# Kernel optimization log

Measured on AMD Instinct MI355X. Metric: run time of the kernel, lower is better.

## Reference

```python
import jax, jax.numpy as jnp
import numpy as np

PAD = 2  # kernel_height // 2 for kernel_height=5


def earth_pad2d(x, ph, pw):
    # circular pad in longitude (last dim), zero pad in latitude (dim 2)
    if pw > 0:
        x = jnp.concatenate([x[..., -pw:], x, x[..., :pw]], axis=-1)
    if ph > 0:
        x = jnp.pad(x, ((0, 0), (0, 0), (ph, ph), (0, 0)))
    return x


def earth_wrap2d(x, w, pad):
    # fold circular overhang of a transposed-conv output back onto width w
    core = x[..., pad:pad + w]
    rw = x.shape[-1] - pad - w  # right overhang (stride-1... here 1)
    core = core.at[..., :rw].add(x[..., pad + w:])
    core = core.at[..., w - pad:].add(x[..., :pad])
    return core


def _conv(x, w, b, stride):
    # torch Conv2d, weight [Cout, Cin, 1, k], VALID padding, stride (1, stride)
    y = jax.lax.conv_general_dilated(x, w, (1, stride), 'VALID',
                                     dimension_numbers=('NCHW', 'OIHW', 'NCHW'))
    return y + b[None, :, None, None]


def _convT(x, w, stride):
    # torch ConvTranspose2d (no bias), weight [Cin, Cout, 1, k], padding 0
    k = w.shape[-1]
    wr = jnp.transpose(jnp.flip(w, axis=(2, 3)), (1, 0, 2, 3))  # -> [Cout, Cin, 1, k]
    return jax.lax.conv_general_dilated(x, wr, (1, 1),
                                        [(0, 0), (k - 1, k - 1)],
                                        lhs_dilation=(1, stride),
                                        dimension_numbers=('NCHW', 'OIHW', 'NCHW'))


def _edge(x, d, p):
    return x[:, :, -p:, :] if d == 1 else x[:, :, :p, :]


def _set_edge(x, d, p, v):
    return x.at[:, :, -p:, :].set(v) if d == 1 else x.at[:, :, :p, :].set(v)


def _forward(strips, wi, wo):
    strips_pad = [earth_pad2d(s, PAD, PAD) for s in strips]
    # center strip inner edges from the adjacent coarser strips (to_inners[0])
    for d in (-1, 1):
        a = _edge(strips[2 + d], -d, PAD)
        a = _convT(a, wi[0], 2)
        a = earth_wrap2d(a, strips[2].shape[3], 2)
        a = earth_pad2d(a, 0, PAD)
        strips_pad[2] = _set_edge(strips_pad[2], d, PAD, a)
    # outer strips: far edge from next coarser (to_inners), near edge from finer (to_outers)
    for mi in (1, 2):
        for d in (-1, 1):
            idx = 2 + d * mi
            sp = strips_pad[idx]
            if mi + 1 <= 2:
                o = _edge(strips[2 + d * (mi + 1)], -d, PAD)
                o = _convT(o, wi[mi], 2)
                o = earth_wrap2d(o, strips[idx].shape[3], 2)
                o = earth_pad2d(o, 0, PAD)
                sp = _set_edge(sp, d, PAD, o)
            en = _edge(strips[2 + d * (mi - 1)], d, PAD)
            en = earth_pad2d(en, 0, 2)
            en = _conv(en, wo[mi - 1][0], wo[mi - 1][1], 2)
            en = earth_pad2d(en, 0, PAD)
            sp = _set_edge(sp, -d, PAD, en)
            strips_pad[idx] = sp
    return tuple(strips_pad)


def setup_inputs():
    key = jax.random.key(0)
    ks = jax.random.split(key, 11)
    B, C, W = 1, 256, 1440
    shapes = [(B, C, 30, W // 4), (B, C, 60, W // 2), (B, C, 180, W),
              (B, C, 60, W // 2), (B, C, 30, W // 4)]
    d = {}
    for i, sh in enumerate(shapes):
        d['s%d' % i] = jax.random.normal(ks[i], sh, dtype=jnp.float32)
    scale = 0.03
    d['wi0'] = jax.random.normal(ks[5], (C, C, 1, 5), dtype=jnp.float32) * scale
    d['wi1'] = jax.random.normal(ks[6], (C, C, 1, 5), dtype=jnp.float32) * scale
    d['wo0'] = jax.random.normal(ks[7], (C, C, 1, 5), dtype=jnp.float32) * scale
    d['bo0'] = jax.random.normal(ks[8], (C,), dtype=jnp.float32) * 0.01
    d['wo1'] = jax.random.normal(ks[9], (C, C, 1, 5), dtype=jnp.float32) * scale
    d['bo1'] = jax.random.normal(ks[10], (C,), dtype=jnp.float32) * 0.01
    return d


def reference(s0, s1, s2, s3, s4, wi0, wi1, wo0, bo0, wo1, bo1):
    return _forward([s0, s1, s2, s3, s4], [wi0, wi1], [(wo0, bo0), (wo1, bo1)])
```

## Files before the change

### kernel.cpp

```cpp
#include <hip/hip_runtime.h>


struct ConvJob {
  const float* x; const float* wt; const float* bias; float* out;
  int Hin, Win, r0, Hout, Wcore, h0, type, blk_start;
};

struct MegaParams {
  ConvJob j[8];
  const float* in0; const float* in1; const float* in2; const float* in3; const float* in4;
  float* o0; float* o1; float* o2; float* o3; float* o4;
};

struct WTParams { const float* src[4]; float* dst[4]; };

__global__ __launch_bounds__(256) void transpose_all_kernel(WTParams p) {
  int b = blockIdx.x;
  int which = b / 1280;
  int idx = (b - which * 1280) * 256 + threadIdx.x;
  int oc = idx & 255;
  int q = idx >> 8;
  int k = q % 5;
  int ic = q / 5;
  const float* s = p.src[which];
  float v = (which < 2) ? s[(ic * 256 + oc) * 5 + k] : s[(oc * 256 + ic) * 5 + k];
  p.dst[which][idx] = v;
}

template <int H, int W>
__device__ __forceinline__ void copy_strip_rows(const float* __restrict__ in,
                                                float* __restrict__ out,
                                                int lb, int nb, int t) {
  constexpr int WO4 = W / 4 + 1;
  constexpr int NROWS = 256 * H;
  int wave = t >> 6, lane = t & 63;
  for (int row = lb * 4 + wave; row < NROWS; row += nb * 4) {
    int c = row / H;
    const float* src = in + (size_t)row * W;
    float* dst = out + (size_t)(row + c * 4 + 2) * (W + 4);
    for (int w4 = 1 + lane; w4 < WO4 - 1; w4 += 64) {
      const float* p = src + w4 * 4;
      float2 a = *(const float2*)(p - 2);
      float2 b = *(const float2*)(p);
      *(float4*)(dst + w4 * 4) = make_float4(a.x, a.y, b.x, b.y);
    }
    if (lane == 0) {
      float2 E = *(const float2*)(src + W - 2);
      float2 F = *(const float2*)(src);
      float4 v = make_float4(E.x, E.y, F.x, F.y);
      *(float4*)(dst) = v;
      *(float4*)(dst + W) = v;
    }
  }
}

__device__ __forceinline__ void conv_block(const ConvJob jb, int local, int t, float* xs) {
  int tile = local >> 1;
  int r = local & 1;
  const int Win = jb.Win;
  const float* xrow = jb.x + ((size_t)(t * jb.Hin + jb.r0 + r)) * Win;
  const float* wt = jb.wt + t;
  const int Wop = jb.Wcore + 4;
  float* orow = jb.out + ((size_t)(t * jb.Hout + jb.h0 + r)) * Wop;

  if (jb.type == 1) {
    int u0 = tile * 8;
    int cb = 2 * u0 - 2;
#pragma unroll
    for (int cc = 0; cc < 19; ++cc) {
      int col = cb + cc;
      col += (col < 0) ? Win : 0;
      col -= (col >= Win) ? Win : 0;
      xs[cc * 256 + t] = xrow[col];
    }
    __syncthreads();
    float bv = jb.bias[t];
    float acc[8];
#pragma unroll
    for (int i = 0; i < 8; ++i) acc[i] = bv;
    for (int ic0 = 0; ic0 < 256; ic0 += 4) {
      float w[4][5];
#pragma unroll
      for (int i = 0; i < 4; ++i)
#pragma unroll
        for (int k = 0; k < 5; ++k) w[i][k] = wt[((ic0 + i) * 5 + k) * 256];
#pragma unroll
      for (int cc = 0; cc < 19; ++cc) {
        float4 xq = *(const float4*)&xs[cc * 256 + ic0];
#pragma unroll
        for (int i = 0; i < 8; ++i) {
          int k = cc - 2 * i;
          if (k >= 0 && k < 5)
            acc[i] += w[0][k] * xq.x + w[1][k] * xq.y + w[2][k] * xq.z + w[3][k] * xq.w;
        }
      }
    }
#pragma unroll
    for (int i = 0; i < 8; ++i) {
      int g = u0 + i;
      float vv = acc[i];
      orow[2 + g] = vv;
      if (g < 2) orow[jb.Wcore + 2 + g] = vv;
      if (g >= jb.Wcore - 2) orow[g - (jb.Wcore - 2)] = vv;
    }
  } else {
    int m0 = tile * 16;
    int j0 = (m0 >> 1) - 1;
#pragma unroll
    for (int cc = 0; cc < 10; ++cc) {
      int col = j0 + cc;
      col += (col < 0) ? Win : 0;
      col -= (col >= Win) ? Win : 0;
      xs[cc * 256 + t] = xrow[col];
    }
    __syncthreads();
    float acc[16];
#pragma unroll
    for (int i = 0; i < 16; ++i) acc[i] = 0.f;
    for (int ic0 = 0; ic0 < 256; ic0 += 4) {
      float w[4][5];
#pragma unroll
      for (int i = 0; i < 4; ++i)
#pragma unroll
        for (int k = 0; k < 5; ++k) w[i][k] = wt[((ic0 + i) * 5 + k) * 256];
#pragma unroll
      for (int cc = 0; cc < 10; ++cc) {
        float4 xq = *(const float4*)&xs[cc * 256 + ic0];
#pragma unroll
        for (int ml = 0; ml < 16; ++ml) {
          int k = ml + 4 - 2 * cc;
          if (k >= 0 && k < 5)
            acc[ml] += w[0][k] * xq.x + w[1][k] * xq.y + w[2][k] * xq.z + w[3][k] * xq.w;
        }
      }
    }
#pragma unroll
    for (int i = 0; i < 16; ++i) {
      int g = m0 + i;
      float vv = acc[i];
      orow[2 + g] = vv;
      if (g < 2) orow[jb.Wcore + 2 + g] = vv;
      if (g >= jb.Wcore - 2) orow[g - (jb.Wcore - 2)] = vv;
    }
  }
}

__device__ __forceinline__ void conv_dispatch(const MegaParams& p, int u, int t, float* xs) {
  int ji = 0;
#pragma unroll
  for (int i = 1; i < 8; ++i)
    if (u >= p.j[i].blk_start) ji = i;
  conv_block(p.j[ji], u - p.j[ji].blk_start, t, xs);
}

__global__ __launch_bounds__(256, 7) void mega_kernel(MegaParams p) {
  __shared__ float xs[19 * 256];
  int bx = blockIdx.x;
  int t = threadIdx.x;
  if (bx < 540) {
    conv_dispatch(p, bx, t, xs);
    __syncthreads();
    conv_dispatch(p, bx + 540, t, xs);
  } else if (bx < 1410) {
    copy_strip_rows<180, 1440>(p.in2, p.o2, bx - 540, 870, t);
  } else if (bx < 1556) {
    copy_strip_rows<60, 720>(p.in1, p.o1, bx - 1410, 146, t);
  } else if (bx < 1702) {
    copy_strip_rows<60, 720>(p.in3, p.o3, bx - 1556, 146, t);
  } else if (bx < 1740) {
    copy_strip_rows<30, 360>(p.in0, p.o0, bx - 1702, 38, t);
  } else if (bx < 1778) {
    copy_strip_rows<30, 360>(p.in4, p.o4, bx - 1740, 38, t);
  } else {
    int lb = bx - 1778;
    int wave = t >> 6, lane = t & 63;
    for (int row = lb * 4 + wave; row < 1024; row += 24) {
      int strip = row >> 9;
      int cr = row & 511;
      int c = cr >> 1, r = cr & 1;
      float* dst = strip ? p.o4 + (size_t)(c * 34 + 32 + r) * 364
                         : p.o0 + (size_t)(c * 34 + r) * 364;
      for (int w4 = lane; w4 < 91; w4 += 64)
        *(float4*)(dst + w4 * 4) = make_float4(0.f, 0.f, 0.f, 0.f);
    }
  }
}

extern "C" void kernel_launch(void* const* d_in, const int* in_sizes, int n_in,
                              void* d_out, int out_size, void* d_ws, size_t ws_size,
                              hipStream_t stream) {
  const float* s0 = (const float*)d_in[0];
  const float* s1 = (const float*)d_in[1];
  const float* s2 = (const float*)d_in[2];
  const float* s3 = (const float*)d_in[3];
  const float* s4 = (const float*)d_in[4];
  const float* wi0 = (const float*)d_in[5];
  const float* wi1 = (const float*)d_in[6];
  const float* wo0 = (const float*)d_in[7];
  const float* bo0 = (const float*)d_in[8];
  const float* wo1 = (const float*)d_in[9];
  const float* bo1 = (const float*)d_in[10];

  float* out = (float*)d_out;
  float* out0 = out;
  float* out1 = out + 3168256;
  float* out2 = out + 15030272;
  float* out3 = out + 83048448;
  float* out4 = out + 94910464;

  float* wt0 = (float*)d_ws;
  float* wt1 = wt0 + 327680;
  float* wt2 = wt1 + 327680;
  float* wt3 = wt2 + 327680;

  WTParams wp;
  wp.src[0] = wi0; wp.src[1] = wi1; wp.src[2] = wo0; wp.src[3] = wo1;
  wp.dst[0] = wt0; wp.dst[1] = wt1; wp.dst[2] = wt2; wp.dst[3] = wt3;
  transpose_all_kernel<<<5120, 256, 0, stream>>>(wp);

  MegaParams mp;
  mp.j[0] = {s1, wt0, nullptr, out2,  60,  720,  58, 184, 1440,   0, 0,   0};
  mp.j[1] = {s3, wt0, nullptr, out2,  60,  720,   0, 184, 1440, 182, 0, 180};
  mp.j[2] = {s0, wt1, nullptr, out1,  30,  360,  28,  64,  720,   0, 0, 360};
  mp.j[3] = {s4, wt1, nullptr, out3,  30,  360,   0,  64,  720,  62, 0, 450};
  mp.j[4] = {s2, wt2, bo0,     out1, 180, 1440,   0,  64,  720,  62, 1, 540};
  mp.j[5] = {s2, wt2, bo0,     out3, 180, 1440, 178,  64,  720,   0, 1, 720};
  mp.j[6] = {s1, wt3, bo1,     out0,  60,  720,   0,  34,  360,  32, 1, 900};
  mp.j[7] = {s3, wt3, bo1,     out4,  60,  720,  58,  34,  360,   0, 1, 990};
  mp.in0 = s0; mp.in1 = s1; mp.in2 = s2; mp.in3 = s3; mp.in4 = s4;
  mp.o0 = out0; mp.o1 = out1; mp.o2 = out2; mp.o3 = out3; mp.o4 = out4;

  mega_kernel<<<1784, 256, 0, stream>>>(mp);
}
```

Baseline: 312.0 us.

## Drop weight transpose kernel, read original weight layouts with register prefetch

Removes the separate weight-transpose launch. The conv code now reads the original PyTorch weight layouts directly: float4 loads of each thread's contiguous per-output-channel row for the forward conv, and strided loads for the transposed conv. Weights for the next input-channel group are prefetched into registers. Conv types are split into two specialized functions with static dispatch, the grid shrinks from 1784 to 1024 blocks, and occupancy hints drop from 7 to 4. Uncoalesced per-thread weight loads and fewer copy blocks may hurt bandwidth in exchange for saving a launch.

After: 577.3 us. +85.1%, slower.

```diff
diff --git a/kernel.cpp b/kernel.cpp
--- a/kernel.cpp
+++ b/kernel.cpp
@@ -2,8 +2,8 @@
 
 
 struct ConvJob {
-  const float* x; const float* wt; const float* bias; float* out;
-  int Hin, Win, r0, Hout, Wcore, h0, type, blk_start;
+  const float* x; const float* w; const float* bias; float* out;
+  int Hin, Win, r0, Hout, Wcore, h0, blk_start;
 };
 
 struct MegaParams {
@@ -11,21 +11,6 @@
   const float* in0; const float* in1; const float* in2; const float* in3; const float* in4;
   float* o0; float* o1; float* o2; float* o3; float* o4;
 };
-
-struct WTParams { const float* src[4]; float* dst[4]; };
-
-__global__ __launch_bounds__(256) void transpose_all_kernel(WTParams p) {
-  int b = blockIdx.x;
-  int which = b / 1280;
-  int idx = (b - which * 1280) * 256 + threadIdx.x;
-  int oc = idx & 255;
-  int q = idx >> 8;
-  int k = q % 5;
-  int ic = q / 5;
-  const float* s = p.src[which];
-  float v = (which < 2) ? s[(ic * 256 + oc) * 5 + k] : s[(oc * 256 + ic) * 5 + k];
-  p.dst[which][idx] = v;
-}
 
 template <int H, int W>
 __device__ __forceinline__ void copy_strip_rows(const float* __restrict__ in,
@@ -38,6 +23,7 @@
     int c = row / H;
     const float* src = in + (size_t)row * W;
     float* dst = out + (size_t)(row + c * 4 + 2) * (W + 4);
+#pragma unroll 2
     for (int w4 = 1 + lane; w4 < WO4 - 1; w4 += 64) {
       const float* p = src + w4 * 4;
       float2 a = *(const float2*)(p - 2);
@@ -54,127 +40,147 @@
   }
 }
 
-__device__ __forceinline__ void conv_block(const ConvJob jb, int local, int t, float* xs) {
+__device__ __forceinline__ void conv_fwd(const ConvJob jb, int local, int t, float* xs) {
   int tile = local >> 1;
   int r = local & 1;
   const int Win = jb.Win;
   const float* xrow = jb.x + ((size_t)(t * jb.Hin + jb.r0 + r)) * Win;
-  const float* wt = jb.wt + t;
+  const float* wbase = jb.w + (size_t)t * 1280;
   const int Wop = jb.Wcore + 4;
   float* orow = jb.out + ((size_t)(t * jb.Hout + jb.h0 + r)) * Wop;
 
-  if (jb.type == 1) {
-    int u0 = tile * 8;
-    int cb = 2 * u0 - 2;
+  int u0 = tile * 8;
+  int cb = 2 * u0 - 2;
+#pragma unroll
+  for (int cc = 0; cc < 19; ++cc) {
+    int col = cb + cc;
+    col += (col < 0) ? Win : 0;
+    col -= (col >= Win) ? Win : 0;
+    xs[cc * 256 + t] = xrow[col];
+  }
+  __syncthreads();
+  float bv = jb.bias[t];
+  float acc[8];
+#pragma unroll
+  for (int i = 0; i < 8; ++i) acc[i] = bv;
+  float4 wv[5];
+#pragma unroll
+  for (int q = 0; q < 5; ++q) wv[q] = *(const float4*)(wbase + 4 * q);
+  for (int ic0 = 0; ic0 < 256; ic0 += 4) {
+    float4 wn[5];
+    if (ic0 + 4 < 256) {
+      const float* wp = wbase + (ic0 + 4) * 5;
+#pragma unroll
+      for (int q = 0; q < 5; ++q) wn[q] = *(const float4*)(wp + 4 * q);
+    }
+    const float* wf = (const float*)wv;
 #pragma unroll
     for (int cc = 0; cc < 19; ++cc) {
-      int col = cb + cc;
-      col += (col < 0) ? Win : 0;
-      col -= (col >= Win) ? Win : 0;
-      xs[cc * 256 + t] = xrow[col];
-    }
-    __syncthreads();
-    float bv = jb.bias[t];
-    float acc[8];
-#pragma unroll
-    for (int i = 0; i < 8; ++i) acc[i] = bv;
-    for (int ic0 = 0; ic0 < 256; ic0 += 4) {
-      float w[4][5];
+      float4 xq = *(const float4*)&xs[cc * 256 + ic0];
+#pragma unroll
+      for (int i = 0; i < 8; ++i) {
+        int k = cc - 2 * i;
+        if (k >= 0 && k < 5)
+          acc[i] += wf[k] * xq.x + wf[5 + k] * xq.y + wf[10 + k] * xq.z + wf[15 + k] * xq.w;
+      }
+    }
+#pragma unroll
+    for (int q = 0; q < 5; ++q) wv[q] = wn[q];
+  }
+#pragma unroll
+  for (int i = 0; i < 8; ++i) {
+    int g = u0 + i;
+    float vv = acc[i];
+    orow[2 + g] = vv;
+    if (g < 2) orow[jb.Wcore + 2 + g] = vv;
+    if (g >= jb.Wcore - 2) orow[g - (jb.Wcore - 2)] = vv;
+  }
+}
+
+__device__ __forceinline__ void conv_tr(const ConvJob jb, int local, int t, float* xs) {
+  int tile = local >> 1;
+  int r = local & 1;
+  const int Win = jb.Win;
+  const float* xrow = jb.x + ((size_t)(t * jb.Hin + jb.r0 + r)) * Win;
+  const float* wbase = jb.w + (size_t)t * 5;
+  const int Wop = jb.Wcore + 4;
+  float* orow = jb.out + ((size_t)(t * jb.Hout + jb.h0 + r)) * Wop;
+
+  int m0 = tile * 16;
+  int j0 = (m0 >> 1) - 1;
+#pragma unroll
+  for (int cc = 0; cc < 10; ++cc) {
+    int col = j0 + cc;
+    col += (col < 0) ? Win : 0;
+    col -= (col >= Win) ? Win : 0;
+    xs[cc * 256 + t] = xrow[col];
+  }
+  __syncthreads();
+  float acc[16];
+#pragma unroll
+  for (int i = 0; i < 16; ++i) acc[i] = 0.f;
+  float w[20];
+#pragma unroll
+  for (int i = 0; i < 4; ++i)
+#pragma unroll
+    for (int k = 0; k < 5; ++k) w[i * 5 + k] = wbase[(size_t)i * 1280 + k];
+  for (int ic0 = 0; ic0 < 256; ic0 += 4) {
+    float wn[20];
+    if (ic0 + 4 < 256) {
 #pragma unroll
       for (int i = 0; i < 4; ++i)
 #pragma unroll
-        for (int k = 0; k < 5; ++k) w[i][k] = wt[((ic0 + i) * 5 + k) * 256];
-#pragma unroll
-      for (int cc = 0; cc < 19; ++cc) {
-        float4 xq = *(const float4*)&xs[cc * 256 + ic0];
-#pragma unroll
-        for (int i = 0; i < 8; ++i) {
-          int k = cc - 2 * i;
-          if (k >= 0 && k < 5)
-            acc[i] += w[0][k] * xq.x + w[1][k] * xq.y + w[2][k] * xq.z + w[3][k] * xq.w;
-        }
+        for (int k = 0; k < 5; ++k) wn[i * 5 + k] = wbase[(size_t)(ic0 + 4 + i) * 1280 + k];
+    }
+#pragma unroll
+    for (int cc = 0; cc < 10; ++cc) {
+      float4 xq = *(const float4*)&xs[cc * 256 + ic0];
+#pragma unroll
+      for (int ml = 0; ml < 16; ++ml) {
+        int k = ml + 4 - 2 * cc;
+        if (k >= 0 && k < 5)
+          acc[ml] += w[k] * xq.x + w[5 + k] * xq.y + w[10 + k] * xq.z + w[15 + k] * xq.w;
       }
     }
 #pragma unroll
-    for (int i = 0; i < 8; ++i) {
-      int g = u0 + i;
-      float vv = acc[i];
-      orow[2 + g] = vv;
-      if (g < 2) orow[jb.Wcore + 2 + g] = vv;
-      if (g >= jb.Wcore - 2) orow[g - (jb.Wcore - 2)] = vv;
-    }
-  } else {
-    int m0 = tile * 16;
-    int j0 = (m0 >> 1) - 1;
-#pragma unroll
-    for (int cc = 0; cc < 10; ++cc) {
-      int col = j0 + cc;
-      col += (col < 0) ? Win : 0;
-      col -= (col >= Win) ? Win : 0;
-      xs[cc * 256 + t] = xrow[col];
-    }
-    __syncthreads();
-    float acc[16];
-#pragma unroll
-    for (int i = 0; i < 16; ++i) acc[i] = 0.f;
-    for (int ic0 = 0; ic0 < 256; ic0 += 4) {
-      float w[4][5];
-#pragma unroll
-      for (int i = 0; i < 4; ++i)
-#pragma unroll
-        for (int k = 0; k < 5; ++k) w[i][k] = wt[((ic0 + i) * 5 + k) * 256];
-#pragma unroll
-      for (int cc = 0; cc < 10; ++cc) {
-        float4 xq = *(const float4*)&xs[cc * 256 + ic0];
-#pragma unroll
-        for (int ml = 0; ml < 16; ++ml) {
-          int k = ml + 4 - 2 * cc;
-          if (k >= 0 && k < 5)
-            acc[ml] += w[0][k] * xq.x + w[1][k] * xq.y + w[2][k] * xq.z + w[3][k] * xq.w;
-        }
-      }
-    }
-#pragma unroll
-    for (int i = 0; i < 16; ++i) {
-      int g = m0 + i;
-      float vv = acc[i];
-      orow[2 + g] = vv;
-      if (g < 2) orow[jb.Wcore + 2 + g] = vv;
-      if (g >= jb.Wcore - 2) orow[g - (jb.Wcore - 2)] = vv;
-    }
-  }
-}
-
-__device__ __forceinline__ void conv_dispatch(const MegaParams& p, int u, int t, float* xs) {
-  int ji = 0;
-#pragma unroll
-  for (int i = 1; i < 8; ++i)
-    if (u >= p.j[i].blk_start) ji = i;
-  conv_block(p.j[ji], u - p.j[ji].blk_start, t, xs);
-}
-
-__global__ __launch_bounds__(256, 7) void mega_kernel(MegaParams p) {
+    for (int e = 0; e < 20; ++e) w[e] = wn[e];
+  }
+#pragma unroll
+  for (int i = 0; i < 16; ++i) {
+    int g = m0 + i;
+    float vv = acc[i];
+    orow[2 + g] = vv;
+    if (g < 2) orow[jb.Wcore + 2 + g] = vv;
+    if (g >= jb.Wcore - 2) orow[g - (jb.Wcore - 2)] = vv;
+  }
+}
+
+__global__ __launch_bounds__(256, 4) void mega_kernel(MegaParams p) {
   __shared__ float xs[19 * 256];
   int bx = blockIdx.x;
   int t = threadIdx.x;
   if (bx < 540) {
-    conv_dispatch(p, bx, t, xs);
+    int u = bx;
+    int ji = (u >= 450) ? 3 : (u >= 360) ? 2 : (u >= 180) ? 1 : 0;
+    conv_tr(p.j[ji], u - p.j[ji].blk_start, t, xs);
     __syncthreads();
-    conv_dispatch(p, bx + 540, t, xs);
-  } else if (bx < 1410) {
-    copy_strip_rows<180, 1440>(p.in2, p.o2, bx - 540, 870, t);
-  } else if (bx < 1556) {
-    copy_strip_rows<60, 720>(p.in1, p.o1, bx - 1410, 146, t);
-  } else if (bx < 1702) {
-    copy_strip_rows<60, 720>(p.in3, p.o3, bx - 1556, 146, t);
-  } else if (bx < 1740) {
-    copy_strip_rows<30, 360>(p.in0, p.o0, bx - 1702, 38, t);
-  } else if (bx < 1778) {
-    copy_strip_rows<30, 360>(p.in4, p.o4, bx - 1740, 38, t);
+    int u2 = bx + 540;
+    int j2 = (u2 >= 990) ? 7 : (u2 >= 900) ? 6 : (u2 >= 720) ? 5 : 4;
+    conv_fwd(p.j[j2], u2 - p.j[j2].blk_start, t, xs);
+  } else if (bx < 840) {
+    copy_strip_rows<180, 1440>(p.in2, p.o2, bx - 540, 300, t);
+  } else if (bx < 912) {
+    copy_strip_rows<60, 720>(p.in1, p.o1, bx - 840, 72, t);
+  } else if (bx < 984) {
+    copy_strip_rows<60, 720>(p.in3, p.o3, bx - 912, 72, t);
+  } else if (bx < 1002) {
+    copy_strip_rows<30, 360>(p.in0, p.o0, bx - 984, 18, t);
+  } else if (bx < 1020) {
+    copy_strip_rows<30, 360>(p.in4, p.o4, bx - 1002, 18, t);
   } else {
-    int lb = bx - 1778;
+    int lb = bx - 1020;
     int wave = t >> 6, lane = t & 63;
-    for (int row = lb * 4 + wave; row < 1024; row += 24) {
+    for (int row = lb * 4 + wave; row < 1024; row += 16) {
       int strip = row >> 9;
       int cr = row & 511;
       int c = cr >> 1, r = cr & 1;
@@ -208,27 +214,17 @@
   float* out3 = out + 83048448;
   float* out4 = out + 94910464;
 
-  float* wt0 = (float*)d_ws;
-  float* wt1 = wt0 + 327680;
-  float* wt2 = wt1 + 327680;
-  float* wt3 = wt2 + 327680;
-
-  WTParams wp;
-  wp.src[0] = wi0; wp.src[1] = wi1; wp.src[2] = wo0; wp.src[3] = wo1;
-  wp.dst[0] = wt0; wp.dst[1] = wt1; wp.dst[2] = wt2; wp.dst[3] = wt3;
-  transpose_all_kernel<<<5120, 256, 0, stream>>>(wp);
-
   MegaParams mp;
-  mp.j[0] = {s1, wt0, nullptr, out2,  60,  720,  58, 184, 1440,   0, 0,   0};
-  mp.j[1] = {s3, wt0, nullptr, out2,  60,  720,   0, 184, 1440, 182, 0, 180};
-  mp.j[2] = {s0, wt1, nullptr, out1,  30,  360,  28,  64,  720,   0, 0, 360};
-  mp.j[3] = {s4, wt1, nullptr, out3,  30,  360,   0,  64,  720,  62, 0, 450};
-  mp.j[4] = {s2, wt2, bo0,     out1, 180, 1440,   0,  64,  720,  62, 1, 540};
-  mp.j[5] = {s2, wt2, bo0,     out3, 180, 1440, 178,  64,  720,   0, 1, 720};
-  mp.j[6] = {s1, wt3, bo1,     out0,  60,  720,   0,  34,  360,  32, 1, 900};
-  mp.j[7] = {s3, wt3, bo1,     out4,  60,  720,  58,  34,  360,   0, 1, 990};
+  mp.j[0] = {s1, wi0, nullptr, out2,  60,  720,  58, 184, 1440,   0,   0};
+  mp.j[1] = {s3, wi0, nullptr, out2,  60,  720,   0, 184, 1440, 182, 180};
+  mp.j[2] = {s0, wi1, nullptr, out1,  30,  360,  28,  64,  720,   0, 360};
+  mp.j[3] = {s4, wi1, nullptr, out3,  30,  360,   0,  64,  720,  62, 450};
+  mp.j[4] = {s2, wo0, bo0,     out1, 180, 1440,   0,  64,  720,  62, 540};
+  mp.j[5] = {s2, wo0, bo0,     out3, 180, 1440, 178,  64,  720,   0, 720};
+  mp.j[6] = {s1, wo1, bo1,     out0,  60,  720,   0,  34,  360,  32, 900};
+  mp.j[7] = {s3, wo1, bo1,     out4,  60,  720,  58,  34,  360,   0, 990};
   mp.in0 = s0; mp.in1 = s1; mp.in2 = s2; mp.in3 = s3; mp.in4 = s4;
   mp.o0 = out0; mp.o1 = out1; mp.o2 = out2; mp.o3 = out3; mp.o4 = out4;
 
-  mega_kernel<<<1784, 256, 0, stream>>>(mp);
-}
+  mega_kernel<<<1024, 256, 0, stream>>>(mp);
+}
```

## Use atomic work-stealing for copy rows and split conv paths with weight prefetch

Applied to the files above, without the earlier changes.

The copy and zero-fill work moves from fixed per-block assignment to a dynamic queue. Each wave grabs 8 rows at a time from a global atomic counter, which the transpose kernel resets before this kernel runs. Conv blocks join the queue after finishing their two conv tiles, so load balances across the grid. The conv code is split into separate transposed and forward functions with no runtime type branch, and weights for the next channel group are register-prefetched. The grid shrinks to 1024 blocks and launch bounds drop to 4 waves, allowing more registers but lowering occupancy.

Measured after the change: 361.8 us. 16.0% more time.

```diff
diff --git a/kernel.cpp b/kernel.cpp
--- a/kernel.cpp
+++ b/kernel.cpp
@@ -3,18 +3,20 @@
 
 struct ConvJob {
   const float* x; const float* wt; const float* bias; float* out;
-  int Hin, Win, r0, Hout, Wcore, h0, type, blk_start;
+  int Hin, Win, r0, Hout, Wcore, h0, blk_start;
 };
 
 struct MegaParams {
   ConvJob j[8];
   const float* in0; const float* in1; const float* in2; const float* in3; const float* in4;
   float* o0; float* o1; float* o2; float* o3; float* o4;
+  unsigned* ctr;
 };
 
-struct WTParams { const float* src[4]; float* dst[4]; };
+struct WTParams { const float* src[4]; float* dst[4]; unsigned* ctr; };
 
 __global__ __launch_bounds__(256) void transpose_all_kernel(WTParams p) {
+  if (blockIdx.x == 0 && threadIdx.x == 0) *p.ctr = 0u;
   int b = blockIdx.x;
   int which = b / 1280;
   int idx = (b - which * 1280) * 256 + threadIdx.x;
@@ -28,33 +30,44 @@
 }
 
 template <int H, int W>
-__device__ __forceinline__ void copy_strip_rows(const float* __restrict__ in,
-                                                float* __restrict__ out,
-                                                int lb, int nb, int t) {
-  constexpr int WO4 = W / 4 + 1;
-  constexpr int NROWS = 256 * H;
-  int wave = t >> 6, lane = t & 63;
-  for (int row = lb * 4 + wave; row < NROWS; row += nb * 4) {
-    int c = row / H;
-    const float* src = in + (size_t)row * W;
-    float* dst = out + (size_t)(row + c * 4 + 2) * (W + 4);
-    for (int w4 = 1 + lane; w4 < WO4 - 1; w4 += 64) {
-      const float* p = src + w4 * 4;
-      float2 a = *(const float2*)(p - 2);
-      float2 b = *(const float2*)(p);
-      *(float4*)(dst + w4 * 4) = make_float4(a.x, a.y, b.x, b.y);
-    }
-    if (lane == 0) {
-      float2 E = *(const float2*)(src + W - 2);
-      float2 F = *(const float2*)(src);
-      float4 v = make_float4(E.x, E.y, F.x, F.y);
-      *(float4*)(dst) = v;
-      *(float4*)(dst + W) = v;
-    }
-  }
-}
-
-__device__ __forceinline__ void conv_block(const ConvJob jb, int local, int t, float* xs) {
+__device__ __forceinline__ void copy_row(const float* __restrict__ in,
+                                         float* __restrict__ out, int rl, int lane) {
+  int c = rl / H;
+  const float* src = in + (size_t)rl * W;
+  float* dst = out + (size_t)(rl + c * 4 + 2) * (W + 4);
+  for (int w4 = 1 + lane; w4 < W / 4; w4 += 64) {
+    const float* q = src + w4 * 4;
+    float2 a = *(const float2*)(q - 2);
+    float2 b = *(const float2*)(q);
+    *(float4*)(dst + w4 * 4) = make_float4(a.x, a.y, b.x, b.y);
+  }
+  if (lane == 0) {
+    float2 E = *(const float2*)(src + W - 2);
+    float2 F = *(const float2*)(src);
+    float4 v = make_float4(E.x, E.y, F.x, F.y);
+    *(float4*)(dst) = v;
+    *(float4*)(dst + W) = v;
+  }
+}
+
+__device__ __forceinline__ void zero_row(const MegaParams& p, int z, int lane) {
+  int strip = z >> 9, cr = z & 511, c = cr >> 1, r = cr & 1;
+  float* dst = strip ? p.o4 + (size_t)(c * 34 + 32 + r) * 364
+                     : p.o0 + (size_t)(c * 34 + r) * 364;
+  for (int w4 = lane; w4 < 91; w4 += 64)
+    *(float4*)(dst + w4 * 4) = make_float4(0.f, 0.f, 0.f, 0.f);
+}
+
+__device__ __forceinline__ void do_row(const MegaParams& p, int gid, int lane) {
+  if (gid < 46080)      copy_row<180, 1440>(p.in2, p.o2, gid, lane);
+  else if (gid < 61440) copy_row<60, 720>(p.in1, p.o1, gid - 46080, lane);
+  else if (gid < 76800) copy_row<60, 720>(p.in3, p.o3, gid - 61440, lane);
+  else if (gid < 84480) copy_row<30, 360>(p.in0, p.o0, gid - 76800, lane);
+  else if (gid < 92160) copy_row<30, 360>(p.in4, p.o4, gid - 84480, lane);
+  else                  zero_row(p, gid - 92160, lane);
+}
+
+__device__ __forceinline__ void conv_tr(const ConvJob jb, int local, int t, float* xs) {
   int tile = local >> 1;
   int r = local & 1;
   const int Win = jb.Win;
@@ -63,126 +76,124 @@
   const int Wop = jb.Wcore + 4;
   float* orow = jb.out + ((size_t)(t * jb.Hout + jb.h0 + r)) * Wop;
 
-  if (jb.type == 1) {
-    int u0 = tile * 8;
-    int cb = 2 * u0 - 2;
+  int m0 = tile * 16;
+  int j0 = (m0 >> 1) - 1;
+#pragma unroll
+  for (int cc = 0; cc < 10; ++cc) {
+    int col = j0 + cc;
+    col += (col < 0) ? Win : 0;
+    col -= (col >= Win) ? Win : 0;
+    xs[cc * 256 + t] = xrow[col];
+  }
+  __syncthreads();
+  float acc[16];
+#pragma unroll
+  for (int i = 0; i < 16; ++i) acc[i] = 0.f;
+  float w[20], wn[20];
+#pragma unroll
+  for (int e = 0; e < 20; ++e) w[e] = wt[e * 256];
+  for (int ic0 = 0; ic0 < 256; ic0 += 4) {
+    if (ic0 + 4 < 256) {
+#pragma unroll
+      for (int e = 0; e < 20; ++e) wn[e] = wt[(size_t)((ic0 + 4) * 5 + e) * 256];
+    }
+#pragma unroll
+    for (int cc = 0; cc < 10; ++cc) {
+      float4 xq = *(const float4*)&xs[cc * 256 + ic0];
+#pragma unroll
+      for (int ml = 0; ml < 16; ++ml) {
+        int k = ml + 4 - 2 * cc;
+        if (k >= 0 && k < 5)
+          acc[ml] += w[k] * xq.x + w[5 + k] * xq.y + w[10 + k] * xq.z + w[15 + k] * xq.w;
+      }
+    }
+#pragma unroll
+    for (int e = 0; e < 20; ++e) w[e] = wn[e];
+  }
+#pragma unroll
+  for (int i = 0; i < 16; ++i) {
+    int g = m0 + i;
+    float vv = acc[i];
+    orow[2 + g] = vv;
+    if (g < 2) orow[jb.Wcore + 2 + g] = vv;
+    if (g >= jb.Wcore - 2) orow[g - (jb.Wcore - 2)] = vv;
+  }
+}
+
+__device__ __forceinline__ void conv_fwd(const ConvJob jb, int local, int t, float* xs) {
+  int tile = local >> 1;
+  int r = local & 1;
+  const int Win = jb.Win;
+  const float* xrow = jb.x + ((size_t)(t * jb.Hin + jb.r0 + r)) * Win;
+  const float* wt = jb.wt + t;
+  const int Wop = jb.Wcore + 4;
+  float* orow = jb.out + ((size_t)(t * jb.Hout + jb.h0 + r)) * Wop;
+
+  int u0 = tile * 8;
+  int cb = 2 * u0 - 2;
+#pragma unroll
+  for (int cc = 0; cc < 19; ++cc) {
+    int col = cb + cc;
+    col += (col < 0) ? Win : 0;
+    col -= (col >= Win) ? Win : 0;
+    xs[cc * 256 + t] = xrow[col];
+  }
+  __syncthreads();
+  float bv = jb.bias[t];
+  float acc[8];
+#pragma unroll
+  for (int i = 0; i < 8; ++i) acc[i] = bv;
+  float w[20], wn[20];
+#pragma unroll
+  for (int e = 0; e < 20; ++e) w[e] = wt[e * 256];
+  for (int ic0 = 0; ic0 < 256; ic0 += 4) {
+    if (ic0 + 4 < 256) {
+#pragma unroll
+      for (int e = 0; e < 20; ++e) wn[e] = wt[(size_t)((ic0 + 4) * 5 + e) * 256];
+    }
 #pragma unroll
     for (int cc = 0; cc < 19; ++cc) {
-      int col = cb + cc;
-      col += (col < 0) ? Win : 0;
-      col -= (col >= Win) ? Win : 0;
-      xs[cc * 256 + t] = xrow[col];
-    }
-    __syncthreads();
-    float bv = jb.bias[t];
-    float acc[8];
-#pragma unroll
-    for (int i = 0; i < 8; ++i) acc[i] = bv;
-    for (int ic0 = 0; ic0 < 256; ic0 += 4) {
-      float w[4][5];
-#pragma unroll
-      for (int i = 0; i < 4; ++i)
-#pragma unroll
-        for (int k = 0; k < 5; ++k) w[i][k] = wt[((ic0 + i) * 5 + k) * 256];
-#pragma unroll
-      for (int cc = 0; cc < 19; ++cc) {
-        float4 xq = *(const float4*)&xs[cc * 256 + ic0];
-#pragma unroll
-        for (int i = 0; i < 8; ++i) {
-          int k = cc - 2 * i;
-          if (k >= 0 && k < 5)
-            acc[i] += w[0][k] * xq.x + w[1][k] * xq.y + w[2][k] * xq.z + w[3][k] * xq.w;
-        }
+      float4 xq = *(const float4*)&xs[cc * 256 + ic0];
+#pragma unroll
+      for (int i = 0; i < 8; ++i) {
+        int k = cc - 2 * i;
+        if (k >= 0 && k < 5)
+          acc[i] += w[k] * xq.x + w[5 + k] * xq.y + w[10 + k] * xq.z + w[15 + k] * xq.w;
       }
     }
 #pragma unroll
-    for (int i = 0; i < 8; ++i) {
-      int g = u0 + i;
-      float vv = acc[i];
-      orow[2 + g] = vv;
-      if (g < 2) orow[jb.Wcore + 2 + g] = vv;
-      if (g >= jb.Wcore - 2) orow[g - (jb.Wcore - 2)] = vv;
-    }
-  } else {
-    int m0 = tile * 16;
-    int j0 = (m0 >> 1) - 1;
-#pragma unroll
-    for (int cc = 0; cc < 10; ++cc) {
-      int col = j0 + cc;
-      col += (col < 0) ? Win : 0;
-      col -= (col >= Win) ? Win : 0;
-      xs[cc * 256 + t] = xrow[col];
-    }
-    __syncthreads();
-    float acc[16];
-#pragma unroll
-    for (int i = 0; i < 16; ++i) acc[i] = 0.f;
-    for (int ic0 = 0; ic0 < 256; ic0 += 4) {
-      float w[4][5];
-#pragma unroll
-      for (int i = 0; i < 4; ++i)
-#pragma unroll
-        for (int k = 0; k < 5; ++k) w[i][k] = wt[((ic0 + i) * 5 + k) * 256];
-#pragma unroll
-      for (int cc = 0; cc < 10; ++cc) {
-        float4 xq = *(const float4*)&xs[cc * 256 + ic0];
-#pragma unroll
-        for (int ml = 0; ml < 16; ++ml) {
-          int k = ml + 4 - 2 * cc;
-          if (k >= 0 && k < 5)
-            acc[ml] += w[0][k] * xq.x + w[1][k] * xq.y + w[2][k] * xq.z + w[3][k] * xq.w;
-        }
-      }
-    }
-#pragma unroll
-    for (int i = 0; i < 16; ++i) {
-      int g = m0 + i;
-      float vv = acc[i];
-      orow[2 + g] = vv;
-      if (g < 2) orow[jb.Wcore + 2 + g] = vv;
-      if (g >= jb.Wcore - 2) orow[g - (jb.Wcore - 2)] = vv;
-    }
-  }
-}
-
-__device__ __forceinline__ void conv_dispatch(const MegaParams& p, int u, int t, float* xs) {
-  int ji = 0;
-#pragma unroll
-  for (int i = 1; i < 8; ++i)
-    if (u >= p.j[i].blk_start) ji = i;
-  conv_block(p.j[ji], u - p.j[ji].blk_start, t, xs);
-}
-
-__global__ __launch_bounds__(256, 7) void mega_kernel(MegaParams p) {
+    for (int e = 0; e < 20; ++e) w[e] = wn[e];
+  }
+#pragma unroll
+  for (int i = 0; i < 8; ++i) {
+    int g = u0 + i;
+    float vv = acc[i];
+    orow[2 + g] = vv;
+    if (g < 2) orow[jb.Wcore + 2 + g] = vv;
+    if (g >= jb.Wcore - 2) orow[g - (jb.Wcore - 2)] = vv;
+  }
+}
+
+__global__ __launch_bounds__(256, 4) void mega_kernel(MegaParams p) {
   __shared__ float xs[19 * 256];
   int bx = blockIdx.x;
   int t = threadIdx.x;
   if (bx < 540) {
-    conv_dispatch(p, bx, t, xs);
+    int ji = (bx >= 450) ? 3 : (bx >= 360) ? 2 : (bx >= 180) ? 1 : 0;
+    conv_tr(p.j[ji], bx - p.j[ji].blk_start, t, xs);
     __syncthreads();
-    conv_dispatch(p, bx + 540, t, xs);
-  } else if (bx < 1410) {
-    copy_strip_rows<180, 1440>(p.in2, p.o2, bx - 540, 870, t);
-  } else if (bx < 1556) {
-    copy_strip_rows<60, 720>(p.in1, p.o1, bx - 1410, 146, t);
-  } else if (bx < 1702) {
-    copy_strip_rows<60, 720>(p.in3, p.o3, bx - 1556, 146, t);
-  } else if (bx < 1740) {
-    copy_strip_rows<30, 360>(p.in0, p.o0, bx - 1702, 38, t);
-  } else if (bx < 1778) {
-    copy_strip_rows<30, 360>(p.in4, p.o4, bx - 1740, 38, t);
-  } else {
-    int lb = bx - 1778;
-    int wave = t >> 6, lane = t & 63;
-    for (int row = lb * 4 + wave; row < 1024; row += 24) {
-      int strip = row >> 9;
-      int cr = row & 511;
-      int c = cr >> 1, r = cr & 1;
-      float* dst = strip ? p.o4 + (size_t)(c * 34 + 32 + r) * 364
-                         : p.o0 + (size_t)(c * 34 + r) * 364;
-      for (int w4 = lane; w4 < 91; w4 += 64)
-        *(float4*)(dst + w4 * 4) = make_float4(0.f, 0.f, 0.f, 0.f);
-    }
+    int u2 = bx + 540;
+    int j2 = (u2 >= 990) ? 7 : (u2 >= 900) ? 6 : (u2 >= 720) ? 5 : 4;
+    conv_fwd(p.j[j2], u2 - p.j[j2].blk_start, t, xs);
+  }
+  int lane = t & 63;
+  for (;;) {
+    int g = 0;
+    if (lane == 0) g = (int)atomicAdd(p.ctr, 1u);
+    g = __shfl(g, 0, 64);
+    if (g >= 11648) break;
+    int base = g * 8;
+    for (int r = 0; r < 8; ++r) do_row(p, base + r, lane);
   }
 }
 
@@ -208,7 +219,8 @@
   float* out3 = out + 83048448;
   float* out4 = out + 94910464;
 
-  float* wt0 = (float*)d_ws;
+  unsigned* ctr = (unsigned*)d_ws;
+  float* wt0 = (float*)d_ws + 16;
   float* wt1 = wt0 + 327680;
   float* wt2 = wt1 + 327680;
   float* wt3 = wt2 + 327680;
@@ -216,19 +228,21 @@
   WTParams wp;
   wp.src[0] = wi0; wp.src[1] = wi1; wp.src[2] = wo0; wp.src[3] = wo1;
   wp.dst[0] = wt0; wp.dst[1] = wt1; wp.dst[2] = wt2; wp.dst[3] = wt3;
+  wp.ctr = ctr;
   transpose_all_kernel<<<5120, 256, 0, stream>>>(wp);
 
   MegaParams mp;
-  mp.j[0] = {s1, wt0, nullptr, out2,  60,  720,  58, 184, 1440,   0, 0,   0};
-  mp.j[1] = {s3, wt0, nullptr, out2,  60,  720,   0, 184, 1440, 182, 0, 180};
-  mp.j[2] = {s0, wt1, nullptr, out1,  30,  360,  28,  64,  720,   0, 0, 360};
-  mp.j[3] = {s4, wt1, nullptr, out3,  30,  360,   0,  64,  720,  62, 0, 450};
-  mp.j[4] = {s2, wt2, bo0,     out1, 180, 1440,   0,  64,  720,  62, 1, 540};
-  mp.j[5] = {s2, wt2, bo0,     out3, 180, 1440, 178,  64,  720,   0, 1, 720};
-  mp.j[6] = {s1, wt3, bo1,     out0,  60,  720,   0,  34,  360,  32, 1, 900};
-  mp.j[7] = {s3, wt3, bo1,     out4,  60,  720,  58,  34,  360,   0, 1, 990};
+  mp.j[0] = {s1, wt0, nullptr, out2,  60,  720,  58, 184, 1440,   0,   0};
+  mp.j[1] = {s3, wt0, nullptr, out2,  60,  720,   0, 184, 1440, 182, 180};
+  mp.j[2] = {s0, wt1, nullptr, out1,  30,  360,  28,  64,  720,   0, 360};
+  mp.j[3] = {s4, wt1, nullptr, out3,  30,  360,   0,  64,  720,  62, 450};
+  mp.j[4] = {s2, wt2, bo0,     out1, 180, 1440,   0,  64,  720,  62, 540};
+  mp.j[5] = {s2, wt2, bo0,     out3, 180, 1440, 178,  64,  720,   0, 720};
+  mp.j[6] = {s1, wt3, bo1,     out0,  60,  720,   0,  34,  360,  32, 900};
+  mp.j[7] = {s3, wt3, bo1,     out4,  60,  720,  58,  34,  360,   0, 990};
   mp.in0 = s0; mp.in1 = s1; mp.in2 = s2; mp.in3 = s3; mp.in4 = s4;
   mp.o0 = out0; mp.o1 = out1; mp.o2 = out2; mp.o3 = out3; mp.o4 = out4;
-
-  mega_kernel<<<1784, 256, 0, stream>>>(mp);
-}
+  mp.ctr = ctr;
+
+  mega_kernel<<<1024, 256, 0, stream>>>(mp);
+}
```
